# Kernel optimization log

Hardware: AMD Instinct MI355X
Metric: run time of the kernel (lower is better)

## Reference

```python
import jax, jax.numpy as jnp
import numpy as np
import math

SLEEP_DIM = 1024
BRAIN_DIM = 512
N_HEADS = 8
D_K = SLEEP_DIM // N_HEADS
N_S = 2048
N_C = 4096
LN_EPS = 1e-5


def setup_inputs() -> dict:
    key = jax.random.key(0)
    ks = jax.random.split(key, 9)
    s = 0.02  # weight init scale
    return {
        "H_S": jax.random.normal(ks[0], (N_S, SLEEP_DIM), dtype=jnp.float32),
        "H_C": jax.random.normal(ks[1], (N_C, BRAIN_DIM), dtype=jnp.float32),
        "G_glyph": jax.random.uniform(ks[2], (N_S, N_C), dtype=jnp.float32),
        "W_Q": jax.random.normal(ks[3], (SLEEP_DIM, SLEEP_DIM), dtype=jnp.float32) * s,
        "W_K": jax.random.normal(ks[4], (SLEEP_DIM, BRAIN_DIM), dtype=jnp.float32) * s,
        "W_V": jax.random.normal(ks[5], (SLEEP_DIM, BRAIN_DIM), dtype=jnp.float32) * s,
        "W_O": jax.random.normal(ks[6], (SLEEP_DIM, SLEEP_DIM), dtype=jnp.float32) * s,
        "b_O": jnp.zeros((SLEEP_DIM,), dtype=jnp.float32),
        "ln_gamma": jnp.ones((SLEEP_DIM,), dtype=jnp.float32),
        "ln_beta": jnp.zeros((SLEEP_DIM,), dtype=jnp.float32),
    }


def reference(H_S, H_C, G_glyph, W_Q, W_K, W_V, W_O, b_O, ln_gamma, ln_beta):
    # projections (torch Linear: x @ W.T)
    Q = (H_S @ W_Q.T).reshape(N_S, N_HEADS, D_K)   # (N_S, H, d_k)
    K = (H_C @ W_K.T).reshape(N_C, N_HEADS, D_K)   # (N_C, H, d_k)
    V = (H_C @ W_V.T).reshape(N_C, N_HEADS, D_K)   # (N_C, H, d_k)

    # scores: (N_S, N_C, H), scaled then multiplicatively gated per (s, c) pair
    scores = jnp.einsum("shd,chd->sch", Q, K) / math.sqrt(D_K)
    scores = scores * G_glyph[:, :, None]

    # softmax over keys (dim=1 of (N_S, N_C, H)); dropout is identity at eval
    attn = jax.nn.softmax(scores, axis=1)

    # weighted value sum, merge heads
    H_new = jnp.einsum("sch,chd->shd", attn, V).reshape(N_S, SLEEP_DIM)
    H_new = H_new @ W_O.T + b_O

    # residual + LayerNorm
    x = H_new + H_S
    mu = jnp.mean(x, axis=-1, keepdims=True)
    var = jnp.var(x, axis=-1, keepdims=True)
    out = (x - mu) / jnp.sqrt(var + LN_EPS) * ln_gamma + ln_beta
    return out, attn.mean(-1)
```

## Files before the change

kernel.cpp:

```cpp
#include <hip/hip_runtime.h>
#include <hip/hip_bf16.h>

#define NS 2048
#define NC 4096
#define SD 1024
#define BD 512
#define NH 8
#define DK 128
#define CSPLIT 4

typedef __bf16 bf16;
typedef __bf16 bf16x8 __attribute__((ext_vector_type(8)));
typedef __bf16 bf16x4 __attribute__((ext_vector_type(4)));
typedef float f32x4 __attribute__((ext_vector_type(4)));
typedef unsigned u32x4 __attribute__((ext_vector_type(4)));

__device__ __forceinline__ bf16 f2bf(float f) { return (bf16)f; }
__device__ __forceinline__ bf16x8 ld8(const bf16* p) { return *(const bf16x8*)p; }
__device__ __forceinline__ f32x4 mfma16(bf16x8 a, bf16x8 b, f32x4 c) {
  return __builtin_amdgcn_mfma_f32_16x16x32_bf16(a, b, c, 0, 0, 0);
}
__device__ __forceinline__ unsigned pkbf(float lo, float hi) {
  unsigned short a = __builtin_bit_cast(unsigned short, (bf16)lo);
  unsigned short b = __builtin_bit_cast(unsigned short, (bf16)hi);
  return (unsigned)a | ((unsigned)b << 16);
}

__global__ void k_cast_all(const float* __restrict__ HS, const float* __restrict__ HC,
                           const float* __restrict__ WQ, const float* __restrict__ WK,
                           const float* __restrict__ WV, const float* __restrict__ WO,
                           const float* __restrict__ G,
                           bf16* __restrict__ HSb, bf16* __restrict__ HCb,
                           bf16* __restrict__ WQb, bf16* __restrict__ WKb,
                           bf16* __restrict__ WVb, bf16* __restrict__ WOb,
                           bf16* __restrict__ Gb) {
  const int n0 = NS * SD / 4, n1 = NC * BD / 4, n2 = SD * SD / 4, n3 = SD * BD / 4;
  const int n4 = SD * BD / 4, n5 = SD * SD / 4, n6 = NS * NC / 4;
  const int total = n0 + n1 + n2 + n3 + n4 + n5 + n6;
  int i = blockIdx.x * blockDim.x + threadIdx.x;
  const int stride = gridDim.x * blockDim.x;
  for (; i < total; i += stride) {
    const float* s; bf16* d; int off = i;
    if (off < n0) { s = HS; d = HSb; }
    else { off -= n0;
      if (off < n1) { s = HC; d = HCb; }
      else { off -= n1;
        if (off < n2) { s = WQ; d = WQb; }
        else { off -= n2;
          if (off < n3) { s = WK; d = WKb; }
          else { off -= n3;
            if (off < n4) { s = WV; d = WVb; }
            else { off -= n4;
              if (off < n5) { s = WO; d = WOb; }
              else { off -= n5; s = G; d = Gb; }
            }
          }
        }
      }
    }
    float4 v = ((const float4*)s)[off];
    bf16x4 o;
    o[0] = f2bf(v.x); o[1] = f2bf(v.y); o[2] = f2bf(v.z); o[3] = f2bf(v.w);
    ((bf16x4*)d)[off] = o;
  }
}

template <typename CT>
__global__ __launch_bounds__(256) void k_gemm64(const bf16* __restrict__ A,
                                                const bf16* __restrict__ B,
                                                CT* __restrict__ C,
                                                int M, int N, int K) {
  __shared__ bf16 As[64 * 64];
  __shared__ bf16 Bs[64 * 64];
  const int tid = threadIdx.x;
  const int l = tid & 63, w = tid >> 6;
  const int g = l >> 4, r15 = l & 15;
  const int m0 = blockIdx.y * 64, n0 = blockIdx.x * 64;
  const int wm = (w >> 1) * 32, wn = (w & 1) * 32;
  f32x4 acc[2][2] = {};
  for (int k0 = 0; k0 < K; k0 += 64) {
    __syncthreads();
#pragma unroll
    for (int i = 0; i < 2; i++) {
      int slot = tid + i * 256;
      int row = slot >> 3, cp = slot & 7;
      int gc = cp ^ (row & 7);
      *(uint4*)(As + slot * 8) = *(const uint4*)(A + (size_t)(m0 + row) * K + k0 + gc * 8);
    }
#pragma unroll
    for (int i = 0; i < 2; i++) {
      int slot = tid + i * 256;
      int row = slot >> 3, cp = slot & 7;
      int gc = cp ^ (row & 7);
      *(uint4*)(Bs + slot * 8) = *(const uint4*)(B + (size_t)(n0 + row) * K + k0 + gc * 8);
    }
    __syncthreads();
#pragma unroll
    for (int kk = 0; kk < 2; kk++) {
      bf16x8 af[2], bfr[2];
#pragma unroll
      for (int mi = 0; mi < 2; mi++) {
        int row = wm + mi * 16 + r15;
        int cidx = (kk * 4 + g) ^ (row & 7);
        af[mi] = *(const bf16x8*)(As + row * 64 + cidx * 8);
      }
#pragma unroll
      for (int ni = 0; ni < 2; ni++) {
        int row = wn + ni * 16 + r15;
        int cidx = (kk * 4 + g) ^ (row & 7);
        bfr[ni] = *(const bf16x8*)(Bs + row * 64 + cidx * 8);
      }
#pragma unroll
      for (int mi = 0; mi < 2; mi++)
#pragma unroll
        for (int ni = 0; ni < 2; ni++)
          acc[mi][ni] = mfma16(af[mi], bfr[ni], acc[mi][ni]);
    }
  }
#pragma unroll
  for (int mi = 0; mi < 2; mi++)
#pragma unroll
    for (int ni = 0; ni < 2; ni++)
#pragma unroll
      for (int rr = 0; rr < 4; rr++) {
        int mrow = m0 + wm + mi * 16 + g * 4 + rr;
        int ncol = n0 + wn + ni * 16 + r15;
        float v = acc[mi][ni][rr];
        if constexpr (sizeof(CT) == 4) C[(size_t)mrow * N + ncol] = v;
        else                           C[(size_t)mrow * N + ncol] = f2bf(v);
      }
}

__global__ __launch_bounds__(256) void k_transpose(const bf16* __restrict__ V, bf16* __restrict__ Vt) {
  __shared__ bf16 tile[32][33];
  const int t = threadIdx.x;
  const int col = t & 31, r0 = t >> 5;
  const int cbase = blockIdx.y * 32;
  const int dbase = blockIdx.x * 32;
#pragma unroll
  for (int i = 0; i < 4; i++) {
    int r = r0 + i * 8;
    tile[r][col] = V[(size_t)(cbase + r) * SD + dbase + col];
  }
  __syncthreads();
#pragma unroll
  for (int i = 0; i < 4; i++) {
    int r = r0 + i * 8;
    Vt[(size_t)(dbase + r) * NC + cbase + col] = tile[col][r];
  }
}

__global__ __launch_bounds__(256, 4) void k_attn3(const bf16* __restrict__ Q, const bf16* __restrict__ Km,
                                                  const bf16* __restrict__ Vt, const bf16* __restrict__ Gb,
                                                  float* __restrict__ psum_part, bf16* __restrict__ Opart) {
  __shared__ bf16 Kl[64 * 128];
  __shared__ bf16 Vl[128 * 64];
  const int tid = threadIdx.x, l = tid & 63, w = tid >> 6, g = l >> 4, r15 = l & 15;
  const int s0 = blockIdx.x * 64;
  const int h = blockIdx.y, hoff = h * DK;
  const int ch = blockIdx.z, cbase = ch * (NC / CSPLIT);
  const int srow = s0 + w * 16 + r15;
  const float scale = 0.08838834764831845f;
  char* KlB = (char*)Kl;
  char* VlB = (char*)Vl;
  const int swz = r15 & 7;

  bf16x8 qf[4];
#pragma unroll
  for (int kk = 0; kk < 4; kk++)
    qf[kk] = ld8(Q + (size_t)srow * SD + hoff + kk * 32 + g * 8);

  f32x4 oacc[8] = {};
  float psum = 0.f;

  const int krow0 = tid >> 4, ksl = tid & 15;
  const int vrow0 = tid >> 3, vsl = tid & 7;
  uint4 kreg[4], vreg[4];
  auto loadstep = [&](int cb) {
#pragma unroll
    for (int i = 0; i < 4; i++)
      kreg[i] = *(const uint4*)(Km + (size_t)(cb + krow0 + i * 16) * SD + hoff + ksl * 8);
#pragma unroll
    for (int i = 0; i < 4; i++)
      vreg[i] = *(const uint4*)(Vt + (size_t)(hoff + vrow0 + i * 32) * NC + cb + vsl * 8);
  };
  loadstep(cbase);

  const int NT = NC / CSPLIT / 64;
  for (int t = 0; t < NT; ++t) {
    const int cb = cbase + t * 64;
    __syncthreads();
#pragma unroll
    for (int i = 0; i < 4; i++) {
      int row = krow0 + i * 16;
      *(uint4*)(KlB + row * 256 + ((ksl ^ (row & 7)) << 4)) = kreg[i];
    }
#pragma unroll
    for (int i = 0; i < 4; i++) {
      int row = vrow0 + i * 32;
      *(uint4*)(VlB + row * 128 + ((vsl ^ (row & 7)) << 4)) = vreg[i];
    }
    __syncthreads();
    uint2 gcur[4];
#pragma unroll
    for (int cs = 0; cs < 4; cs++)
      gcur[cs] = *(const uint2*)(Gb + (size_t)srow * NC + cb + cs * 16 + g * 4);
    if (t < NT - 1) loadstep(cb + 64);
#pragma unroll
    for (int kc = 0; kc < 2; ++kc) {
      unsigned va0, va1, vb0, vb1;
#pragma unroll
      for (int cs2 = 0; cs2 < 2; ++cs2) {
        const int csub = kc * 2 + cs2;
        bf16x8 kf[4];
#pragma unroll
        for (int kk = 0; kk < 4; kk++)
          kf[kk] = *(const bf16x8*)(KlB + (csub * 16 + r15) * 256 + (((kk * 4 + g) ^ swz) << 4));
        f32x4 a = {0.f, 0.f, 0.f, 0.f};
#pragma unroll
        for (int kk = 0; kk < 4; kk++) a = mfma16(kf[kk], qf[kk], a);
        bf16x4 gb4 = __builtin_bit_cast(bf16x4, gcur[csub]);
        float p0 = __expf(a[0] * scale * (float)gb4[0]);
        float p1 = __expf(a[1] * scale * (float)gb4[1]);
        float p2 = __expf(a[2] * scale * (float)gb4[2]);
        float p3 = __expf(a[3] * scale * (float)gb4[3]);
        psum += (p0 + p1) + (p2 + p3);
        if (cs2 == 0) { va0 = pkbf(p0, p1); va1 = pkbf(p2, p3); }
        else          { vb0 = pkbf(p0, p1); vb1 = pkbf(p2, p3); }
      }
      const bool glow = (g < 2);
      unsigned sa = glow ? vb0 : va0, sb = glow ? vb1 : va1;
      unsigned e0 = (unsigned)__shfl_xor((int)sa, 32);
      unsigned e1 = (unsigned)__shfl_xor((int)sb, 32);
      unsigned p00 = glow ? va0 : e0, p01 = glow ? va1 : e1;
      unsigned p10 = glow ? e0 : vb0, p11 = glow ? e1 : vb1;
      const bool ge = ((g & 1) == 0);
      unsigned t0 = ge ? p10 : p00, t1 = ge ? p11 : p01;
      unsigned f0e = (unsigned)__shfl_xor((int)t0, 16);
      unsigned f1e = (unsigned)__shfl_xor((int)t1, 16);
      u32x4 fv;
      fv[0] = ge ? p00 : f0e;
      fv[1] = ge ? p01 : f1e;
      fv[2] = ge ? f0e : p10;
      fv[3] = ge ? f1e : p11;
      bf16x8 pf = __builtin_bit_cast(bf16x8, fv);
#pragma unroll
      for (int nf = 0; nf < 8; ++nf) {
        bf16x8 vf = *(const bf16x8*)(VlB + (nf * 16 + r15) * 128 + (((kc * 4 + g) ^ swz) << 4));
        oacc[nf] = mfma16(vf, pf, oacc[nf]);
      }
    }
  }
  float ps = psum;
  ps += __shfl_xor(ps, 16);
  ps += __shfl_xor(ps, 32);
  if (g == 0) psum_part[((size_t)ch * NS + srow) * NH + h] = ps;

  __syncthreads();
  char* Sw = KlB + w * 4096;
#pragma unroll
  for (int nf = 0; nf < 8; ++nf) {
    uint2 pk2;
    pk2.x = pkbf(oacc[nf][0], oacc[nf][1]);
    pk2.y = pkbf(oacc[nf][2], oacc[nf][3]);
    *(uint2*)(Sw + r15 * 256 + ((nf * 32 + g * 8) ^ (swz << 4))) = pk2;
  }
  __syncthreads();
  const int sr = l >> 2;
#pragma unroll
  for (int p = 0; p < 4; ++p) {
    int cc = (l & 3) + p * 4;
    uint4 v = *(const uint4*)(Sw + sr * 256 + ((cc * 16) ^ ((sr & 7) << 4)));
    *(uint4*)(Opart + ((size_t)ch * NS + s0 + w * 16 + sr) * SD + hoff + cc * 8) = v;
  }
}

__global__ __launch_bounds__(256) void k_combine(const float* __restrict__ psum_part,
                                                 const bf16* __restrict__ Opart,
                                                 bf16* __restrict__ Hat, float* __restrict__ inv_l) {
  __shared__ float il_s[NH];
  const int row = blockIdx.x, t = threadIdx.x;
  if (t < NH) {
    float s = 0.f;
#pragma unroll
    for (int ch = 0; ch < CSPLIT; ch++) s += psum_part[((size_t)ch * NS + row) * NH + t];
    float iv = 1.0f / s;
    il_s[t] = iv;
    inv_l[(size_t)row * NH + t] = iv;
  }
  __syncthreads();
  const int d0 = t * 4;
  float acc[4] = {0.f, 0.f, 0.f, 0.f};
#pragma unroll
  for (int ch = 0; ch < CSPLIT; ch++) {
    bf16x4 v = *(const bf16x4*)(Opart + ((size_t)ch * NS + row) * SD + d0);
#pragma unroll
    for (int j = 0; j < 4; j++) acc[j] += (float)v[j];
  }
  float iv = il_s[d0 >> 7];
  bf16 ob[4] __attribute__((aligned(8)));
#pragma unroll
  for (int j = 0; j < 4; j++) ob[j] = f2bf(acc[j] * iv);
  *(uint2*)(Hat + (size_t)row * SD + d0) = *(const uint2*)ob;
}

__global__ __launch_bounds__(256) void k_mean2(const bf16* __restrict__ Q, const bf16* __restrict__ Km,
                                               const bf16* __restrict__ Gb, const float* __restrict__ inv_l,
                                               float* __restrict__ out_mean) {
  __shared__ bf16 Klm[64 * 128];
  __shared__ bf16 Qlm[64 * 128];
  __shared__ float ilv_s[64][NH];
  const int tid = threadIdx.x;
  const int l = tid & 63, w = tid >> 6;
  const int g = l >> 4, r15 = l & 15;
  const int ws = w >> 1, wc = w & 1;
  const int c0 = blockIdx.x * 64, s0 = blockIdx.y * 64;
  const float scale = 0.08838834764831845f;
  const int swz = r15 & 7;
  char* KB = (char*)Klm;
  char* QB = (char*)Qlm;
  const int row0 = tid >> 4, sl = tid & 15;

  for (int i = tid; i < 64 * NH; i += 256)
    ilv_s[i >> 3][i & 7] = inv_l[(size_t)(s0 + (i >> 3)) * NH + (i & 7)];

  uint2 gvb[2][2];
#pragma unroll
  for (int smi = 0; smi < 2; smi++)
#pragma unroll
    for (int csub = 0; csub < 2; csub++)
      gvb[smi][csub] = *(const uint2*)(Gb + (size_t)(s0 + ws * 32 + smi * 16 + r15) * NC +
                                       c0 + wc * 32 + csub * 16 + g * 4);

  f32x4 macc[2][2] = {};
  uint4 kreg[4], qreg[4];
  auto loadh = [&](int h) {
#pragma unroll
    for (int i = 0; i < 4; i++)
      kreg[i] = *(const uint4*)(Km + (size_t)(c0 + row0 + i * 16) * SD + h * DK + sl * 8);
#pragma unroll
    for (int i = 0; i < 4; i++)
      qreg[i] = *(const uint4*)(Q + (size_t)(s0 + row0 + i * 16) * SD + h * DK + sl * 8);
  };
  loadh(0);
  for (int h = 0; h < NH; ++h) {
    __syncthreads();
#pragma unroll
    for (int i = 0; i < 4; i++) {
      int row = row0 + i * 16;
      *(uint4*)(KB + row * 256 + ((sl ^ (row & 7)) << 4)) = kreg[i];
    }
#pragma unroll
    for (int i = 0; i < 4; i++) {
      int row = row0 + i * 16;
      *(uint4*)(QB + row * 256 + ((sl ^ (row & 7)) << 4)) = qreg[i];
    }
    __syncthreads();
    if (h < NH - 1) loadh(h + 1);
    bf16x8 kf[2][4], qfr[2][4];
#pragma unroll
    for (int csub = 0; csub < 2; csub++)
#pragma unroll
      for (int kk = 0; kk < 4; kk++)
        kf[csub][kk] = *(const bf16x8*)(KB + (wc * 32 + csub * 16 + r15) * 256 + (((kk * 4 + g) ^ swz) << 4));
#pragma unroll
    for (int smi = 0; smi < 2; smi++)
#pragma unroll
      for (int kk = 0; kk < 4; kk++)
        qfr[smi][kk] = *(const bf16x8*)(QB + (ws * 32 + smi * 16 + r15) * 256 + (((kk * 4 + g) ^ swz) << 4));
    float ilv[2];
#pragma unroll
    for (int smi = 0; smi < 2; smi++)
      ilv[smi] = ilv_s[ws * 32 + smi * 16 + r15][h];
#pragma unroll
    for (int smi = 0; smi < 2; smi++)
#pragma unroll
      for (int csub = 0; csub < 2; csub++) {
        f32x4 a = {0.f, 0.f, 0.f, 0.f};
#pragma unroll
        for (int kk = 0; kk < 4; kk++) a = mfma16(kf[csub][kk], qfr[smi][kk], a);
        bf16x4 gb4 = __builtin_bit_cast(bf16x4, gvb[smi][csub]);
        macc[smi][csub][0] += __expf(a[0] * scale * (float)gb4[0]) * ilv[smi];
        macc[smi][csub][1] += __expf(a[1] * scale * (float)gb4[1]) * ilv[smi];
        macc[smi][csub][2] += __expf(a[2] * scale * (float)gb4[2]) * ilv[smi];
        macc[smi][csub][3] += __expf(a[3] * scale * (float)gb4[3]) * ilv[smi];
      }
  }
#pragma unroll
  for (int smi = 0; smi < 2; smi++)
#pragma unroll
    for (int csub = 0; csub < 2; csub++) {
      int srow = s0 + ws * 32 + smi * 16 + r15;
      float4 o;
      o.x = macc[smi][csub][0] * 0.125f;
      o.y = macc[smi][csub][1] * 0.125f;
      o.z = macc[smi][csub][2] * 0.125f;
      o.w = macc[smi][csub][3] * 0.125f;
      *(float4*)(out_mean + (size_t)srow * NC + c0 + wc * 32 + csub * 16 + g * 4) = o;
    }
}

__global__ __launch_bounds__(256) void k_ln(const float* __restrict__ Op, const float* __restrict__ HS,
                                            const float* __restrict__ bO, const float* __restrict__ gamma,
                                            const float* __restrict__ beta, float* __restrict__ out) {
  __shared__ float rs[4][2];
  const int row = blockIdx.x, t = threadIdx.x;
  const int l = t & 63, w = t >> 6;
  float4 xo = *(const float4*)(Op + (size_t)row * SD + t * 4);
  float4 hs = *(const float4*)(HS + (size_t)row * SD + t * 4);
  float4 bo = *(const float4*)(bO + t * 4);
  float x[4] = {xo.x + hs.x + bo.x, xo.y + hs.y + bo.y,
                xo.z + hs.z + bo.z, xo.w + hs.w + bo.w};
  float s = x[0] + x[1] + x[2] + x[3];
  float q = x[0] * x[0] + x[1] * x[1] + x[2] * x[2] + x[3] * x[3];
#pragma unroll
  for (int m = 1; m < 64; m <<= 1) { s += __shfl_xor(s, m); q += __shfl_xor(q, m); }
  if (l == 0) { rs[w][0] = s; rs[w][1] = q; }
  __syncthreads();
  s = rs[0][0] + rs[1][0] + rs[2][0] + rs[3][0];
  q = rs[0][1] + rs[1][1] + rs[2][1] + rs[3][1];
  float mean = s * (1.0f / SD);
  float var = q * (1.0f / SD) - mean * mean;
  float rstd = rsqrtf(var + 1e-5f);
  float4 gm = *(const float4*)(gamma + t * 4);
  float4 bt = *(const float4*)(beta + t * 4);
  float4 o;
  o.x = (x[0] - mean) * rstd * gm.x + bt.x;
  o.y = (x[1] - mean) * rstd * gm.y + bt.y;
  o.z = (x[2] - mean) * rstd * gm.z + bt.z;
  o.w = (x[3] - mean) * rstd * gm.w + bt.w;
  *(float4*)(out + (size_t)row * SD + t * 4) = o;
}

extern "C" void kernel_launch(void* const* d_in, const int* in_sizes, int n_in,
                              void* d_out, int out_size, void* d_ws, size_t ws_size,
                              hipStream_t stream) {
  const float* H_S = (const float*)d_in[0];
  const float* H_C = (const float*)d_in[1];
  const float* G   = (const float*)d_in[2];
  const float* W_Q = (const float*)d_in[3];
  const float* W_K = (const float*)d_in[4];
  const float* W_V = (const float*)d_in[5];
  const float* W_O = (const float*)d_in[6];
  const float* b_O = (const float*)d_in[7];
  const float* gam = (const float*)d_in[8];
  const float* bet = (const float*)d_in[9];
  float* out = (float*)d_out;
  float* out_mean = out + (size_t)NS * SD;

  char* p = (char*)d_ws;
  auto alloc = [&](size_t bytes) { char* r = p; p += (bytes + 255) & ~(size_t)255; return r; };
  char* region0 = alloc((size_t)20 << 20);
  bf16* HSb = (bf16*)region0;
  bf16* HCb = (bf16*)(region0 + ((size_t)4 << 20));
  bf16* WQb = (bf16*)(region0 + ((size_t)8 << 20));
  bf16* WKb = (bf16*)(region0 + ((size_t)10 << 20));
  bf16* WVb = (bf16*)(region0 + ((size_t)11 << 20));
  bf16* Vb  = (bf16*)(region0 + ((size_t)12 << 20));
  bf16* Opart = (bf16*)region0;
  bf16* WOb = (bf16*)alloc((size_t)SD * SD * 2);
  bf16* Qb  = (bf16*)alloc((size_t)NS * SD * 2);
  bf16* Kb  = (bf16*)alloc((size_t)NC * SD * 2);
  bf16* Vtb = (bf16*)alloc((size_t)SD * NC * 2);
  bf16* Hat = (bf16*)alloc((size_t)NS * SD * 2);
  float* Opj = (float*)alloc((size_t)NS * SD * 4);
  float* invl = (float*)alloc((size_t)NS * NH * 4);
  float* psum_part = (float*)alloc((size_t)CSPLIT * NS * NH * 4);
  bf16* Gb = (bf16*)alloc((size_t)NS * NC * 2);

  k_cast_all<<<2048, 256, 0, stream>>>(H_S, H_C, W_Q, W_K, W_V, W_O, G,
                                       HSb, HCb, WQb, WKb, WVb, WOb, Gb);

  k_gemm64<bf16><<<dim3(SD / 64, NS / 64), 256, 0, stream>>>(HSb, WQb, Qb, NS, SD, SD);
  k_gemm64<bf16><<<dim3(SD / 64, NC / 64), 256, 0, stream>>>(HCb, WKb, Kb, NC, SD, BD);
  k_gemm64<bf16><<<dim3(SD / 64, NC / 64), 256, 0, stream>>>(HCb, WVb, Vb, NC, SD, BD);
  k_transpose<<<dim3(SD / 32, NC / 32), 256, 0, stream>>>(Vb, Vtb);

  k_attn3<<<dim3(NS / 64, NH, CSPLIT), 256, 0, stream>>>(Qb, Kb, Vtb, Gb, psum_part, Opart);
  k_combine<<<NS, 256, 0, stream>>>(psum_part, Opart, Hat, invl);
  k_mean2<<<dim3(NC / 64, NS / 64), 256, 0, stream>>>(Qb, Kb, Gb, invl, out_mean);

  k_gemm64<float><<<dim3(SD / 64, NS / 64), 256, 0, stream>>>(Hat, WOb, Opj, NS, SD, SD);
  k_ln<<<NS, 256, 0, stream>>>(Opj, H_S, b_O, gam, bet, out);
}
```

Measured before the change: 516.0 us.

## Remap block IDs for XCD locality, relayout Opart per head, stage mean stores

Block indices in the attention and mean kernels are remapped so that consecutive work items land on the same XCD (bid&7 interleave), which should improve L2 reuse of shared K/V/Q tiles. Opart is now stored per (chunk, head) with contiguous DK-wide rows, and the combine kernel reads it in that layout. The mean kernel stages its output tile through shared memory so global stores become full-row coalesced float4 writes. The attention kernel also drops its min-blocks occupancy hint, which changes the register budget and may lower occupancy.

Result: no change. 521.8 us (+1.1%).

```diff
diff --git a/kernel.cpp b/kernel.cpp
--- a/kernel.cpp
+++ b/kernel.cpp
@@ -150,15 +150,17 @@
   }
 }
 
-__global__ __launch_bounds__(256, 4) void k_attn3(const bf16* __restrict__ Q, const bf16* __restrict__ Km,
-                                                  const bf16* __restrict__ Vt, const bf16* __restrict__ Gb,
-                                                  float* __restrict__ psum_part, bf16* __restrict__ Opart) {
+__global__ __launch_bounds__(256) void k_attn3(const bf16* __restrict__ Q, const bf16* __restrict__ Km,
+                                               const bf16* __restrict__ Vt, const bf16* __restrict__ Gb,
+                                               float* __restrict__ psum_part, bf16* __restrict__ Opart) {
   __shared__ bf16 Kl[64 * 128];
   __shared__ bf16 Vl[128 * 64];
   const int tid = threadIdx.x, l = tid & 63, w = tid >> 6, g = l >> 4, r15 = l & 15;
-  const int s0 = blockIdx.x * 64;
-  const int h = blockIdx.y, hoff = h * DK;
-  const int ch = blockIdx.z, cbase = ch * (NC / CSPLIT);
+  const int bid = blockIdx.x + 32 * (blockIdx.y + 8 * blockIdx.z);
+  const int work = (bid & 7) * 128 + (bid >> 3);
+  const int s0 = (work & 31) * 64;
+  const int h = (work >> 5) & 7, hoff = h * DK;
+  const int ch = work >> 8, cbase = ch * (NC / CSPLIT);
   const int srow = s0 + w * 16 + r15;
   const float scale = 0.08838834764831845f;
   char* KlB = (char*)Kl;
@@ -271,7 +273,7 @@
   for (int p = 0; p < 4; ++p) {
     int cc = (l & 3) + p * 4;
     uint4 v = *(const uint4*)(Sw + sr * 256 + ((cc * 16) ^ ((sr & 7) << 4)));
-    *(uint4*)(Opart + ((size_t)ch * NS + s0 + w * 16 + sr) * SD + hoff + cc * 8) = v;
+    *(uint4*)(Opart + ((size_t)(ch * NH + h) * NS + s0 + w * 16 + sr) * DK + cc * 8) = v;
   }
 }
 
@@ -290,14 +292,16 @@
   }
   __syncthreads();
   const int d0 = t * 4;
+  const int hh = t >> 5;
+  const int dk = d0 & 127;
   float acc[4] = {0.f, 0.f, 0.f, 0.f};
 #pragma unroll
   for (int ch = 0; ch < CSPLIT; ch++) {
-    bf16x4 v = *(const bf16x4*)(Opart + ((size_t)ch * NS + row) * SD + d0);
+    bf16x4 v = *(const bf16x4*)(Opart + ((size_t)(ch * NH + hh) * NS + row) * DK + dk);
 #pragma unroll
     for (int j = 0; j < 4; j++) acc[j] += (float)v[j];
   }
-  float iv = il_s[d0 >> 7];
+  float iv = il_s[hh];
   bf16 ob[4] __attribute__((aligned(8)));
 #pragma unroll
   for (int j = 0; j < 4; j++) ob[j] = f2bf(acc[j] * iv);
@@ -307,22 +311,23 @@
 __global__ __launch_bounds__(256) void k_mean2(const bf16* __restrict__ Q, const bf16* __restrict__ Km,
                                                const bf16* __restrict__ Gb, const float* __restrict__ inv_l,
                                                float* __restrict__ out_mean) {
-  __shared__ bf16 Klm[64 * 128];
-  __shared__ bf16 Qlm[64 * 128];
-  __shared__ float ilv_s[64][NH];
+  __shared__ char smem[32768 + 64 * NH * 4];
+  char* KB = smem;
+  char* QB = smem + 16384;
+  float* ilv_s = (float*)(smem + 32768);
   const int tid = threadIdx.x;
   const int l = tid & 63, w = tid >> 6;
   const int g = l >> 4, r15 = l & 15;
   const int ws = w >> 1, wc = w & 1;
-  const int c0 = blockIdx.x * 64, s0 = blockIdx.y * 64;
+  const int bid = blockIdx.x + 64 * blockIdx.y;
+  const int work = (bid & 7) * 256 + (bid >> 3);
+  const int c0 = (work & 63) * 64, s0 = (work >> 6) * 64;
   const float scale = 0.08838834764831845f;
   const int swz = r15 & 7;
-  char* KB = (char*)Klm;
-  char* QB = (char*)Qlm;
   const int row0 = tid >> 4, sl = tid & 15;
 
   for (int i = tid; i < 64 * NH; i += 256)
-    ilv_s[i >> 3][i & 7] = inv_l[(size_t)(s0 + (i >> 3)) * NH + (i & 7)];
+    ilv_s[i] = inv_l[(size_t)(s0 + (i >> 3)) * NH + (i & 7)];
 
   uint2 gvb[2][2];
 #pragma unroll
@@ -371,7 +376,7 @@
     float ilv[2];
 #pragma unroll
     for (int smi = 0; smi < 2; smi++)
-      ilv[smi] = ilv_s[ws * 32 + smi * 16 + r15][h];
+      ilv[smi] = ilv_s[(ws * 32 + smi * 16 + r15) * NH + h];
 #pragma unroll
     for (int smi = 0; smi < 2; smi++)
 #pragma unroll
@@ -386,18 +391,30 @@
         macc[smi][csub][3] += __expf(a[3] * scale * (float)gb4[3]) * ilv[smi];
       }
   }
+  __syncthreads();
+  float* Tb = (float*)smem;
 #pragma unroll
   for (int smi = 0; smi < 2; smi++)
 #pragma unroll
     for (int csub = 0; csub < 2; csub++) {
-      int srow = s0 + ws * 32 + smi * 16 + r15;
+      int rr = ws * 32 + smi * 16 + r15;
+      int cc = wc * 32 + csub * 16 + g * 4;
       float4 o;
       o.x = macc[smi][csub][0] * 0.125f;
       o.y = macc[smi][csub][1] * 0.125f;
       o.z = macc[smi][csub][2] * 0.125f;
       o.w = macc[smi][csub][3] * 0.125f;
-      *(float4*)(out_mean + (size_t)srow * NC + c0 + wc * 32 + csub * 16 + g * 4) = o;
-    }
+      *(float4*)(Tb + rr * 68 + cc) = o;
+    }
+  __syncthreads();
+  {
+    const int r = tid >> 2, q = tid & 3;
+#pragma unroll
+    for (int j = 0; j < 4; j++) {
+      float4 v = *(const float4*)(Tb + r * 68 + q * 16 + j * 4);
+      *(float4*)(out_mean + (size_t)(s0 + r) * NC + c0 + q * 16 + j * 4) = v;
+    }
+  }
 }
 
 __global__ __launch_bounds__(256) void k_ln(const float* __restrict__ Op, const float* __restrict__ HS,
```
